# Kernel tuning notes

Hardware: AMD Instinct MI355X
Metric: run time of the kernel (lower is better)

Reference implementation:

```python
import jax, jax.numpy as jnp
import numpy as np

N, D, H, E = 8192, 1024, 4096, 8


def setup_inputs() -> dict:
    key = jax.random.key(0)
    ks = jax.random.split(key, 5)
    s_in = 1.0 / np.sqrt(D)
    s_h = 1.0 / np.sqrt(H)
    return {
        "x": jax.random.normal(ks[0], (N, D), dtype=jnp.float32),
        "Wg": jax.random.normal(ks[1], (D, E), dtype=jnp.float32) * s_in,
        "bg": jnp.zeros((E,), dtype=jnp.float32),
        "W1": jax.random.normal(ks[2], (E, D, H), dtype=jnp.float32) * s_in,
        "b1": jnp.zeros((E, H), dtype=jnp.float32),
        "W2": jax.random.normal(ks[3], (E, H, D), dtype=jnp.float32) * s_h,
        "b2": jnp.zeros((E, D), dtype=jnp.float32),
    }


def reference(x, Wg, bg, W1, b1, W2, b2):
    # gate: softmax linear router -> weights [N, E]
    weights = jax.nn.softmax(x @ Wg + bg, axis=-1)
    # all experts, batched GEMMs: h [N, E, H]
    h = jax.nn.relu(jnp.einsum("nd,edh->neh", x, W1) + b1)  # Dropout is identity at inference
    outputs = jnp.einsum("neh,ehd->ned", h, W2) + b2         # [N, E, D]
    # weighted combine over experts
    return jnp.einsum("ne,ned->nd", weights, outputs)
```

## Files before the change

kernel.cpp:

```cpp
#include <hip/hip_runtime.h>
#include <hip/hip_bf16.h>

#define DDIM 1024
#define HDIM 4096
#define NEXP 8
#define NROW 8192
#define KPAIR 8192

typedef __attribute__((ext_vector_type(8))) short s16x8;
typedef __attribute__((ext_vector_type(4))) float f32x4;

using bf16 = __hip_bfloat16;

__device__ __forceinline__ void gload16(const bf16* g, bf16* lds) {
    __builtin_amdgcn_global_load_lds(
        (const __attribute__((address_space(1))) unsigned int*)g,
        (__attribute__((address_space(3))) unsigned int*)lds,
        16, 0, 0);
}

template <int N>
__device__ __forceinline__ void wait_vmcnt() {
    if constexpr (N == 6)      asm volatile("s_waitcnt vmcnt(6)" ::: "memory");
    else if constexpr (N == 3) asm volatile("s_waitcnt vmcnt(3)" ::: "memory");
    else                       asm volatile("s_waitcnt vmcnt(0)" ::: "memory");
}

__global__ void cvtgate_kernel(const float* __restrict__ x, const float* __restrict__ Wg,
                               const float* __restrict__ bg, const float* __restrict__ b2,
                               bf16* __restrict__ xb, float* __restrict__ wts,
                               float* __restrict__ out) {
    int wave = threadIdx.x >> 6, lane = threadIdx.x & 63;
    int n = blockIdx.x * 4 + wave;
    const float* xr = x + (size_t)n * DDIM;
    bf16* xbr = xb + (size_t)n * DDIM;
    float acc[NEXP] = {0.f, 0.f, 0.f, 0.f, 0.f, 0.f, 0.f, 0.f};
#pragma unroll
    for (int j = 0; j < 4; ++j) {
        int d0 = j * 256 + lane * 4;
        float4 v = *(const float4*)&xr[d0];
        union { bf16 b[4]; uint2 u; } pk;
        pk.b[0] = __float2bfloat16(v.x);
        pk.b[1] = __float2bfloat16(v.y);
        pk.b[2] = __float2bfloat16(v.z);
        pk.b[3] = __float2bfloat16(v.w);
        *(uint2*)&xbr[d0] = pk.u;
        const float* w0 = Wg + (size_t)d0 * NEXP;
#pragma unroll
        for (int e = 0; e < NEXP; ++e)
            acc[e] += v.x * w0[e] + v.y * w0[NEXP + e] + v.z * w0[2 * NEXP + e] +
                      v.w * w0[3 * NEXP + e];
    }
#pragma unroll
    for (int off = 32; off > 0; off >>= 1) {
#pragma unroll
        for (int e = 0; e < NEXP; ++e) acc[e] += __shfl_xor(acc[e], off, 64);
    }
    float mx = -1e30f;
#pragma unroll
    for (int e = 0; e < NEXP; ++e) { acc[e] += bg[e]; mx = fmaxf(mx, acc[e]); }
    float s = 0.f;
#pragma unroll
    for (int e = 0; e < NEXP; ++e) { acc[e] = __expf(acc[e] - mx); s += acc[e]; }
    float inv = 1.0f / s;
#pragma unroll
    for (int e = 0; e < NEXP; ++e) acc[e] *= inv;
    if (lane == 0) {
#pragma unroll
        for (int e = 0; e < NEXP; ++e) wts[(size_t)n * NEXP + e] = acc[e];
    }
    float* outr = out + (size_t)n * DDIM;
#pragma unroll
    for (int j = 0; j < 4; ++j) {
        int d0 = j * 256 + lane * 4;
        float4 sum = {0.f, 0.f, 0.f, 0.f};
#pragma unroll
        for (int e = 0; e < NEXP; ++e) {
            float4 bv = *(const float4*)&b2[(size_t)e * DDIM + d0];
            sum.x += acc[e] * bv.x;
            sum.y += acc[e] * bv.y;
            sum.z += acc[e] * bv.z;
            sum.w += acc[e] * bv.w;
        }
        *(float4*)&outr[d0] = sum;
    }
}

__global__ void transpose_pair_kernel(const float* __restrict__ W1s, bf16* __restrict__ W1d,
                                      const float* __restrict__ W2s, bf16* __restrict__ W2d) {
    __shared__ float t[128][65];
    const int z = blockIdx.z;
    const float* src; bf16* dst; int C, ldo, bx, by;
    if (z < 2) {
        src = W1s + (size_t)z * DDIM * HDIM;
        dst = W1d + (size_t)z * HDIM * DDIM;
        C = HDIM; ldo = DDIM;
        bx = blockIdx.x & 31; by = blockIdx.x >> 5;
    } else {
        src = W2s + (size_t)(z - 2) * HDIM * DDIM;
        dst = W2d + (size_t)(z - 2) * HDIM;
        C = DDIM; ldo = KPAIR;
        bx = blockIdx.x & 7; by = blockIdx.x >> 3;
    }
    const int r0 = by * 64, c0 = bx * 128;
    const int tid = threadIdx.x;
    const int lrow = tid >> 5, lc4 = tid & 31;
#pragma unroll
    for (int i = 0; i < 8; ++i) {
        int rr = i * 8 + lrow;
        float4 v = *(const float4*)&src[(size_t)(r0 + rr) * C + c0 + lc4 * 4];
        t[lc4 * 4 + 0][rr] = v.x;
        t[lc4 * 4 + 1][rr] = v.y;
        t[lc4 * 4 + 2][rr] = v.z;
        t[lc4 * 4 + 3][rr] = v.w;
    }
    __syncthreads();
    const int oc = tid >> 3, oj = tid & 7;
#pragma unroll
    for (int i = 0; i < 4; ++i) {
        int c = oc + i * 32;
        union { bf16 b[8]; s16x8 v; } p;
#pragma unroll
        for (int q = 0; q < 8; ++q) p.b[q] = __float2bfloat16(t[c][oj * 8 + q]);
        *(s16x8*)&dst[(size_t)(c0 + c) * ldo + r0 + oj * 8] = p.v;
    }
}

__global__ __launch_bounds__(512, 1) void gemm1(
    const bf16* __restrict__ A, const bf16* __restrict__ BTp, bf16* __restrict__ Hsb,
    const float* __restrict__ b1p, const float* __restrict__ wts,
    int lda, int ldb, int ldc, int NT, int tilesM, int tilesN, int XGN, int e0) {
    constexpr int WROWS = 128;
    constexpr int HALFA = 256 * 32;
    constexpr int HALFB = 256 * 32;
    constexpr int ATOT = 2 * HALFA;
    constexpr int BUFE = ATOT + 2 * HALFB;
    __shared__ __align__(16) bf16 smem[2 * BUFE];

    const int tid = threadIdx.x;
    const int wave = tid >> 6, lane = tid & 63;
    const int wm = wave >> 2, wn = wave & 3;
    const int r = lane & 15, kg = lane >> 4;

    const int eh = blockIdx.x >> 9;
    const int bx = blockIdx.x & 511;
    const bf16* BT = BTp + (size_t)eh * HDIM * DDIM;
    bf16* Cout = Hsb + (size_t)eh * HDIM;
    const float* bias = b1p + (size_t)eh * HDIM;
    const int expert = e0 + eh;

    const int xcd = bx & 7, slot = bx >> 3;
    const int XGM = 8 / XGN;
    const int rm = tilesM / XGM, rn = tilesN / XGN;
    const int g = slot >> 5, u = slot & 31;
    const int gpr = rn >> 3;
    const int gm = (g / gpr) * 4 + (u >> 3);
    const int gn = (g % gpr) * 8 + (u & 7);
    const int tm = (xcd / XGN) * rm + gm;
    const int tn = (xcd % XGN) * rn + gn;

    const bf16* gA = A + (size_t)tm * 256 * lda;
    const bf16* gB = BT + (size_t)tn * 256 * ldb;

    f32x4 acc[8][4];
#pragma unroll
    for (int m = 0; m < 8; ++m)
#pragma unroll
        for (int n = 0; n < 4; ++n) acc[m][n] = (f32x4){0.f, 0.f, 0.f, 0.f};

    auto stageA = [&](int t, int ks) {
        bf16* dst = smem + (t & 1) * BUFE + ks * HALFA;
#pragma unroll
        for (int j = 0; j < 2; ++j) {
            int c = j * 512 + tid;
            int R = c >> 2, kc = (c & 3) ^ ((R >> 1) & 3);
            gload16(gA + (size_t)R * lda + t * 64 + ks * 32 + kc * 8,
                    dst + (j * 512 + wave * 64) * 8);
        }
    };
    auto stageB = [&](int t, int ks) {
        bf16* dst = smem + (t & 1) * BUFE + ATOT + ks * HALFB;
#pragma unroll
        for (int j = 0; j < 2; ++j) {
            int c = j * 512 + tid;
            int R = c >> 2, kc = (c & 3) ^ ((R >> 1) & 3);
            gload16(gB + (size_t)R * ldb + t * 64 + ks * 32 + kc * 8,
                    dst + (j * 512 + wave * 64) * 8);
        }
    };

    s16x8 aLo[4], aHi[4], bb[4];
    auto ldALo = [&](int buf, int ks) {
#pragma unroll
        for (int m = 0; m < 4; ++m) {
            int R = wm * WROWS + m * 16 + r;
            aLo[m] = *(const s16x8*)&smem[buf * BUFE + ks * HALFA + R * 32 +
                                          ((kg ^ ((R >> 1) & 3)) * 8)];
        }
    };
    auto ldAHi = [&](int buf, int ks) {
#pragma unroll
        for (int m = 0; m < 4; ++m) {
            int R = wm * WROWS + 64 + m * 16 + r;
            aHi[m] = *(const s16x8*)&smem[buf * BUFE + ks * HALFA + R * 32 +
                                          ((kg ^ ((R >> 1) & 3)) * 8)];
        }
    };
    auto ldB = [&](int buf, int ks) {
#pragma unroll
        for (int n = 0; n < 4; ++n) {
            int R = wn * 64 + n * 16 + r;
            bb[n] = *(const s16x8*)&smem[buf * BUFE + ATOT + ks * HALFB + R * 32 +
                                         ((kg ^ ((R >> 1) & 3)) * 8)];
        }
    };

    auto mfmaLo = [&]() {
#pragma unroll
        for (int m = 0; m < 4; ++m)
#pragma unroll
            for (int n = 0; n < 4; ++n)
                acc[m][n] = __builtin_amdgcn_mfma_f32_16x16x32_bf16(aLo[m], bb[n], acc[m][n], 0, 0, 0);
    };
    auto mfmaHi = [&]() {
#pragma unroll
        for (int m = 0; m < 4; ++m)
#pragma unroll
            for (int n = 0; n < 4; ++n)
                acc[4 + m][n] = __builtin_amdgcn_mfma_f32_16x16x32_bf16(aHi[m], bb[n], acc[4 + m][n], 0, 0, 0);
    };

    stageA(0, 0); stageB(0, 0); stageA(0, 1); stageB(0, 1);
    wait_vmcnt<0>();
    __builtin_amdgcn_s_barrier();

    for (int t = 0; t < NT; ++t) {
        const int b = t & 1;
        if (t + 1 < NT) { stageA(t + 1, 0); stageB(t + 1, 0); stageA(t + 1, 1); stageB(t + 1, 1); }
        ldB(b, 0); ldALo(b, 0); ldAHi(b, 0);
        asm volatile("s_waitcnt lgkmcnt(4)" ::: "memory");
        __builtin_amdgcn_sched_barrier(0);
        __builtin_amdgcn_s_setprio(1);
        mfmaLo();
        __builtin_amdgcn_s_setprio(0);
        asm volatile("s_waitcnt lgkmcnt(0)" ::: "memory");
        __builtin_amdgcn_sched_barrier(0);
        __builtin_amdgcn_s_setprio(1);
        mfmaHi();
        __builtin_amdgcn_s_setprio(0);
        ldB(b, 1); ldALo(b, 1); ldAHi(b, 1);
        asm volatile("s_waitcnt lgkmcnt(4)" ::: "memory");
        __builtin_amdgcn_sched_barrier(0);
        __builtin_amdgcn_s_setprio(1);
        mfmaLo();
        __builtin_amdgcn_s_setprio(0);
        asm volatile("s_waitcnt lgkmcnt(0)" ::: "memory");
        __builtin_amdgcn_sched_barrier(0);
        __builtin_amdgcn_s_setprio(1);
        mfmaHi();
        __builtin_amdgcn_s_setprio(0);
        if (t + 1 < NT) {
            wait_vmcnt<0>();
            __builtin_amdgcn_s_barrier();
        }
    }

    __builtin_amdgcn_s_barrier();
    bf16* hs = smem;
    const int col0 = tn * 256 + wn * 64;
#pragma unroll
    for (int n = 0; n < 4; ++n) {
        float bv = bias[col0 + n * 16 + r];
        int cl = wn * 64 + n * 16 + r;
#pragma unroll
        for (int mf = 0; mf < 8; ++mf) {
#pragma unroll
            for (int j = 0; j < 4; ++j) {
                int rl = wm * WROWS + (mf >> 2) * 64 + (mf & 3) * 16 + kg * 4 + j;
                float wv = wts[((size_t)tm * 256 + rl) * NEXP + expert];
                float v = acc[mf][n][j] + bv;
                v = v > 0.f ? v : 0.f;
                hs[rl * 256 + (cl ^ ((rl & 7) << 3))] = __float2bfloat16(wv * v);
            }
        }
    }
    __builtin_amdgcn_s_barrier();
    asm volatile("s_waitcnt lgkmcnt(0)" ::: "memory");
    const size_t rbase = (size_t)tm * 256;
    const int cbase = tn * 256;
#pragma unroll
    for (int i2 = 0; i2 < 16; ++i2) {
        int rl = wave * 32 + i2 * 2 + (lane >> 5);
        int c8 = (lane & 31) * 8;
        s16x8 v = *(const s16x8*)&hs[rl * 256 + (c8 ^ ((rl & 7) << 3))];
        *(s16x8*)&Cout[(rbase + rl) * (size_t)ldc + cbase + c8] = v;
    }
}

__global__ __launch_bounds__(256, 2) void gemm2p(
    const bf16* __restrict__ A, const bf16* __restrict__ BT, float* __restrict__ O,
    int lda, int ldb, int ldc, int NT, int tilesM, int tilesN, int XGN) {
    constexpr int HALFA = 128 * 32;
    constexpr int HALFB = 128 * 32;
    constexpr int ATOT = 2 * HALFA;
    constexpr int BUFE = ATOT + 2 * HALFB;
    constexpr int RSTR = 68;
    __shared__ __align__(16) bf16 smem[2 * BUFE];

    const int tid = threadIdx.x;
    const int wave = tid >> 6, lane = tid & 63;
    const int ksw = wave & 1, wn = wave >> 1;
    const int r = lane & 15, kg = lane >> 4;

    const int xcd = blockIdx.x & 7, slot = blockIdx.x >> 3;
    const int XGM = 8 / XGN;
    const int rm = tilesM / XGM, rn = tilesN / XGN;
    const int g = slot >> 5, u = slot & 31;
    const int gpr = rn >> 3;
    const int gm = (g / gpr) * 4 + (u >> 3);
    const int gn = (g % gpr) * 8 + (u & 7);
    const int tm = (xcd / XGN) * rm + gm;
    const int tn = (xcd % XGN) * rn + gn;

    const bf16* gA = A + (size_t)tm * 128 * lda;
    const bf16* gB = BT + (size_t)tn * 128 * ldb;

    f32x4 acc[8][4];
#pragma unroll
    for (int m = 0; m < 8; ++m)
#pragma unroll
        for (int n = 0; n < 4; ++n) acc[m][n] = (f32x4){0.f, 0.f, 0.f, 0.f};

    auto stageA_rh = [&](int t, int rh) {
        bf16* base = smem + (t & 1) * BUFE;
#pragma unroll
        for (int j = 0; j < 2; ++j) {
            int c = j * 256 + tid;
            int Rl = (c >> 2) & 63;
            int R = rh * 64 + Rl;
            int kc = (c & 3) ^ ((R >> 1) & 3);
            gload16(gA + (size_t)R * lda + t * 64 + j * 32 + kc * 8,
                    base + j * HALFA + rh * 2048 + ((c & 255) - lane) * 8 + lane * 8);
        }
    };
    auto stageB = [&](int t) {
        bf16* base = smem + (t & 1) * BUFE + ATOT;
#pragma unroll
        for (int j = 0; j < 4; ++j) {
            int c = j * 256 + tid;
            int ks = c >> 9;
            int R = (c >> 2) & 127;
            int kc = (c & 3) ^ ((R >> 1) & 3);
            gload16(gB + (size_t)R * ldb + t * 64 + ks * 32 + kc * 8,
                    base + ks * HALFB + ((c & 511) - lane) * 8 + lane * 8);
        }
    };

    s16x8 a0[4], a1[4], bfr[4];
    auto ldA0 = [&](int b) {
#pragma unroll
        for (int m = 0; m < 4; ++m) {
            int R = m * 16 + r;
            a0[m] = *(const s16x8*)&smem[b * BUFE + ksw * HALFA + R * 32 +
                                         ((kg ^ ((R >> 1) & 3)) * 8)];
        }
    };
    auto ldA1 = [&](int b) {
#pragma unroll
        for (int m = 0; m < 4; ++m) {
            int R = 64 + m * 16 + r;
            a1[m] = *(const s16x8*)&smem[b * BUFE + ksw * HALFA + R * 32 +
                                         ((kg ^ ((R >> 1) & 3)) * 8)];
        }
    };
    auto ldB = [&](int b) {
#pragma unroll
        for (int n = 0; n < 4; ++n) {
            int R = wn * 64 + n * 16 + r;
            bfr[n] = *(const s16x8*)&smem[b * BUFE + ATOT + ksw * HALFB + R * 32 +
                                          ((kg ^ ((R >> 1) & 3)) * 8)];
        }
    };

    stageA_rh(0, 0); stageA_rh(0, 1); stageB(0);
    wait_vmcnt<0>();
    __builtin_amdgcn_s_barrier();

    for (int t = 0; t < NT; ++t) {
        const int b = t & 1;
        ldB(b); ldA1(b); ldA0(b);
        if (t + 1 < NT) { stageA_rh(t + 1, 0); stageA_rh(t + 1, 1); stageB(t + 1); }
        asm volatile("s_waitcnt lgkmcnt(4)" ::: "memory");
        __builtin_amdgcn_sched_barrier(0);
        __builtin_amdgcn_s_setprio(1);
#pragma unroll
        for (int m = 0; m < 4; ++m)
#pragma unroll
            for (int n = 0; n < 4; ++n)
                acc[4 + m][n] = __builtin_amdgcn_mfma_f32_16x16x32_bf16(a1[m], bfr[n], acc[4 + m][n], 0, 0, 0);
        __builtin_amdgcn_s_setprio(0);
        asm volatile("s_waitcnt lgkmcnt(0)" ::: "memory");
        __builtin_amdgcn_sched_barrier(0);
        __builtin_amdgcn_s_setprio(1);
#pragma unroll
        for (int m = 0; m < 4; ++m)
#pragma unroll
            for (int n = 0; n < 4; ++n)
                acc[m][n] = __builtin_amdgcn_mfma_f32_16x16x32_bf16(a0[m], bfr[n], acc[m][n], 0, 0, 0);
        __builtin_amdgcn_s_setprio(0);
        if (t + 1 < NT) {
            wait_vmcnt<0>();
            __builtin_amdgcn_s_barrier();
        }
    }

    __syncthreads();
    float* red = (float*)smem;
    const int zone = wn * (64 * RSTR);
    const int col0 = tn * 128 + wn * 64;
    const size_t row0 = (size_t)tm * 128;
    if (ksw == 1) {
#pragma unroll
        for (int mq = 0; mq < 4; ++mq)
#pragma unroll
            for (int n = 0; n < 4; ++n) {
                int rl = mq * 16 + kg * 4;
                int cl = n * 16 + r;
#pragma unroll
                for (int j = 0; j < 4; ++j)
                    red[zone + (rl + j) * RSTR + cl] = acc[mq][n][j];
            }
    }
    __syncthreads();
    if (ksw == 0) {
#pragma unroll
        for (int mq = 0; mq < 4; ++mq)
#pragma unroll
            for (int j = 0; j < 4; ++j) {
                int rl = mq * 16 + kg * 4 + j;
                size_t rr = row0 + rl;
#pragma unroll
                for (int n = 0; n < 4; ++n) {
                    int cl = n * 16 + r;
                    O[rr * (size_t)ldc + col0 + cl] += acc[mq][n][j] + red[zone + rl * RSTR + cl];
                }
            }
    }
    __syncthreads();
    if (ksw == 0) {
#pragma unroll
        for (int mq = 0; mq < 4; ++mq)
#pragma unroll
            for (int n = 0; n < 4; ++n) {
                int rl = mq * 16 + kg * 4;
                int cl = n * 16 + r;
#pragma unroll
                for (int j = 0; j < 4; ++j)
                    red[zone + (rl + j) * RSTR + cl] = acc[4 + mq][n][j];
            }
    }
    __syncthreads();
    if (ksw == 1) {
#pragma unroll
        for (int mq = 0; mq < 4; ++mq)
#pragma unroll
            for (int j = 0; j < 4; ++j) {
                int rl = mq * 16 + kg * 4 + j;
                size_t rr = row0 + 64 + rl;
#pragma unroll
                for (int n = 0; n < 4; ++n) {
                    int cl = n * 16 + r;
                    O[rr * (size_t)ldc + col0 + cl] += acc[4 + mq][n][j] + red[zone + rl * RSTR + cl];
                }
            }
    }
}

extern "C" void kernel_launch(void* const* d_in, const int* in_sizes, int n_in,
                              void* d_out, int out_size, void* d_ws, size_t ws_size,
                              hipStream_t stream) {
    const float* x  = (const float*)d_in[0];
    const float* Wg = (const float*)d_in[1];
    const float* bg = (const float*)d_in[2];
    const float* W1 = (const float*)d_in[3];
    const float* b1 = (const float*)d_in[4];
    const float* W2 = (const float*)d_in[5];
    const float* b2 = (const float*)d_in[6];
    float* out = (float*)d_out;

    char* ws = (char*)d_ws;
    bf16* xb   = (bf16*)(ws);
    bf16* W1P  = (bf16*)(ws + (16ull << 20));
    bf16* W2P  = (bf16*)(ws + (32ull << 20));
    bf16* Hs   = (bf16*)(ws + (48ull << 20));
    float* wts = (float*)(ws + (176ull << 20));

    cvtgate_kernel<<<NROW / 4, 256, 0, stream>>>(x, Wg, bg, b2, xb, wts, out);

    for (int p = 0; p < 4; ++p) {
        transpose_pair_kernel<<<dim3(512, 1, 4), 256, 0, stream>>>(
            W1 + (size_t)2 * p * DDIM * HDIM, W1P,
            W2 + (size_t)2 * p * HDIM * DDIM, W2P);
        gemm1<<<1024, 512, 0, stream>>>(
            xb, W1P, Hs, b1 + (size_t)2 * p * HDIM, wts,
            DDIM, DDIM, KPAIR, DDIM / 64, 32, 16, 2, 2 * p);
        gemm2p<<<512, 256, 0, stream>>>(
            Hs, W2P, out, KPAIR, KPAIR, DDIM, KPAIR / 64, 64, 8, 1);
    }
}
```

Baseline: 1.225 ms.

## Restructure gemm1 into 128x128 tiles with intra-block split-K across wave pairs

Replaces the 256x256-tile, 512-thread gemm1 with a 128x128-tile, 256-thread kernel that runs two blocks per CU. Each pair of waves splits the K dimension of every 64-wide step, and the partial sums are reduced through LDS in the epilogue before bias, ReLU and gate scaling. LDS fragment reads now happen before the next global prefetch is issued. This aims to raise occupancy and latency hiding, at the cost of lower arithmetic intensity per tile, more global traffic and an extra LDS reduction with more barriers.

```diff
diff --git a/kernel.cpp b/kernel.cpp
--- a/kernel.cpp
+++ b/kernel.cpp
@@ -126,41 +126,38 @@
     }
 }
 
-__global__ __launch_bounds__(512, 1) void gemm1(
+__global__ __launch_bounds__(256, 2) void gemm1v3(
     const bf16* __restrict__ A, const bf16* __restrict__ BTp, bf16* __restrict__ Hsb,
-    const float* __restrict__ b1p, const float* __restrict__ wts,
-    int lda, int ldb, int ldc, int NT, int tilesM, int tilesN, int XGN, int e0) {
-    constexpr int WROWS = 128;
-    constexpr int HALFA = 256 * 32;
-    constexpr int HALFB = 256 * 32;
+    const float* __restrict__ b1p, const float* __restrict__ wts, int e0) {
+    constexpr int HALFA = 128 * 32;
+    constexpr int HALFB = 128 * 32;
     constexpr int ATOT = 2 * HALFA;
     constexpr int BUFE = ATOT + 2 * HALFB;
+    constexpr int RSTR = 68;
+    constexpr int NT = DDIM / 64;
     __shared__ __align__(16) bf16 smem[2 * BUFE];
 
     const int tid = threadIdx.x;
     const int wave = tid >> 6, lane = tid & 63;
-    const int wm = wave >> 2, wn = wave & 3;
+    const int ksw = wave & 1, wn = wave >> 1;
     const int r = lane & 15, kg = lane >> 4;
 
-    const int eh = blockIdx.x >> 9;
-    const int bx = blockIdx.x & 511;
+    const int eh = blockIdx.x >> 11;
+    const int bx = blockIdx.x & 2047;
     const bf16* BT = BTp + (size_t)eh * HDIM * DDIM;
     bf16* Cout = Hsb + (size_t)eh * HDIM;
     const float* bias = b1p + (size_t)eh * HDIM;
     const int expert = e0 + eh;
 
     const int xcd = bx & 7, slot = bx >> 3;
-    const int XGM = 8 / XGN;
-    const int rm = tilesM / XGM, rn = tilesN / XGN;
     const int g = slot >> 5, u = slot & 31;
-    const int gpr = rn >> 3;
-    const int gm = (g / gpr) * 4 + (u >> 3);
-    const int gn = (g % gpr) * 8 + (u & 7);
-    const int tm = (xcd / XGN) * rm + gm;
-    const int tn = (xcd % XGN) * rn + gn;
-
-    const bf16* gA = A + (size_t)tm * 256 * lda;
-    const bf16* gB = BT + (size_t)tn * 256 * ldb;
+    const int gm = (g >> 1) * 4 + (u >> 3);
+    const int gn = (g & 1) * 8 + (u & 7);
+    const int tm = (xcd >> 1) * 16 + gm;
+    const int tn = (xcd & 1) * 16 + gn;
+
+    const bf16* gA = A + (size_t)tm * 128 * DDIM;
+    const bf16* gB = BT + (size_t)tn * 128 * DDIM;
 
     f32x4 acc[8][4];
 #pragma unroll
@@ -168,96 +165,82 @@
 #pragma unroll
         for (int n = 0; n < 4; ++n) acc[m][n] = (f32x4){0.f, 0.f, 0.f, 0.f};
 
-    auto stageA = [&](int t, int ks) {
-        bf16* dst = smem + (t & 1) * BUFE + ks * HALFA;
+    auto stageA_rh = [&](int t, int rh) {
+        bf16* base = smem + (t & 1) * BUFE;
 #pragma unroll
         for (int j = 0; j < 2; ++j) {
-            int c = j * 512 + tid;
-            int R = c >> 2, kc = (c & 3) ^ ((R >> 1) & 3);
-            gload16(gA + (size_t)R * lda + t * 64 + ks * 32 + kc * 8,
-                    dst + (j * 512 + wave * 64) * 8);
-        }
-    };
-    auto stageB = [&](int t, int ks) {
-        bf16* dst = smem + (t & 1) * BUFE + ATOT + ks * HALFB;
-#pragma unroll
-        for (int j = 0; j < 2; ++j) {
-            int c = j * 512 + tid;
-            int R = c >> 2, kc = (c & 3) ^ ((R >> 1) & 3);
-            gload16(gB + (size_t)R * ldb + t * 64 + ks * 32 + kc * 8,
-                    dst + (j * 512 + wave * 64) * 8);
-        }
-    };
-
-    s16x8 aLo[4], aHi[4], bb[4];
-    auto ldALo = [&](int buf, int ks) {
+            int c = j * 256 + tid;
+            int Rl = (c >> 2) & 63;
+            int R = rh * 64 + Rl;
+            int kc = (c & 3) ^ ((R >> 1) & 3);
+            gload16(gA + (size_t)R * DDIM + t * 64 + j * 32 + kc * 8,
+                    base + j * HALFA + rh * 2048 + ((c & 255) - lane) * 8 + lane * 8);
+        }
+    };
+    auto stageB = [&](int t) {
+        bf16* base = smem + (t & 1) * BUFE + ATOT;
+#pragma unroll
+        for (int j = 0; j < 4; ++j) {
+            int c = j * 256 + tid;
+            int ks = c >> 9;
+            int R = (c >> 2) & 127;
+            int kc = (c & 3) ^ ((R >> 1) & 3);
+            gload16(gB + (size_t)R * DDIM + t * 64 + ks * 32 + kc * 8,
+                    base + ks * HALFB + ((c & 511) - lane) * 8 + lane * 8);
+        }
+    };
+
+    s16x8 a0[4], a1[4], bfr[4];
+    auto ldA0 = [&](int b) {
 #pragma unroll
         for (int m = 0; m < 4; ++m) {
-            int R = wm * WROWS + m * 16 + r;
-            aLo[m] = *(const s16x8*)&smem[buf * BUFE + ks * HALFA + R * 32 +
-                                          ((kg ^ ((R >> 1) & 3)) * 8)];
-        }
-    };
-    auto ldAHi = [&](int buf, int ks) {
+            int R = m * 16 + r;
+            a0[m] = *(const s16x8*)&smem[b * BUFE + ksw * HALFA + R * 32 +
+                                         ((kg ^ ((R >> 1) & 3)) * 8)];
+        }
+    };
+    auto ldA1 = [&](int b) {
 #pragma unroll
         for (int m = 0; m < 4; ++m) {
-            int R = wm * WROWS + 64 + m * 16 + r;
-            aHi[m] = *(const s16x8*)&smem[buf * BUFE + ks * HALFA + R * 32 +
-                                          ((kg ^ ((R >> 1) & 3)) * 8)];
-        }
-    };
-    auto ldB = [&](int buf, int ks) {
+            int R = 64 + m * 16 + r;
+            a1[m] = *(const s16x8*)&smem[b * BUFE + ksw * HALFA + R * 32 +
+                                         ((kg ^ ((R >> 1) & 3)) * 8)];
+        }
+    };
+    auto ldB = [&](int b) {
 #pragma unroll
         for (int n = 0; n < 4; ++n) {
             int R = wn * 64 + n * 16 + r;
-            bb[n] = *(const s16x8*)&smem[buf * BUFE + ATOT + ks * HALFB + R * 32 +
-                                         ((kg ^ ((R >> 1) & 3)) * 8)];
-        }
-    };
-
-    auto mfmaLo = [&]() {
-#pragma unroll
-        for (int m = 0; m < 4; ++m)
-#pragma unroll
-            for (int n = 0; n < 4; ++n)
-                acc[m][n] = __builtin_amdgcn_mfma_f32_16x16x32_bf16(aLo[m], bb[n], acc[m][n], 0, 0, 0);
-    };
-    auto mfmaHi = [&]() {
-#pragma unroll
-        for (int m = 0; m < 4; ++m)
-#pragma unroll
-            for (int n = 0; n < 4; ++n)
-                acc[4 + m][n] = __builtin_amdgcn_mfma_f32_16x16x32_bf16(aHi[m], bb[n], acc[4 + m][n], 0, 0, 0);
-    };
-
-    stageA(0, 0); stageB(0, 0); stageA(0, 1); stageB(0, 1);
+            bfr[n] = *(const s16x8*)&smem[b * BUFE + ATOT + ksw * HALFB + R * 32 +
+                                          ((kg ^ ((R >> 1) & 3)) * 8)];
+        }
+    };
+
+    stageA_rh(0, 0); stageA_rh(0, 1); stageB(0);
     wait_vmcnt<0>();
     __builtin_amdgcn_s_barrier();
 
     for (int t = 0; t < NT; ++t) {
         const int b = t & 1;
-        if (t + 1 < NT) { stageA(t + 1, 0); stageB(t + 1, 0); stageA(t + 1, 1); stageB(t + 1, 1); }
-        ldB(b, 0); ldALo(b, 0); ldAHi(b, 0);
+        ldB(b); ldA1(b); ldA0(b);
+        if (t + 1 < NT) { stageA_rh(t + 1, 0); stageA_rh(t + 1, 1); stageB(t + 1); }
         asm volatile("s_waitcnt lgkmcnt(4)" ::: "memory");
         __builtin_amdgcn_sched_barrier(0);
         __builtin_amdgcn_s_setprio(1);
-        mfmaLo();
+#pragma unroll
+        for (int m = 0; m < 4; ++m)
+#pragma unroll
+            for (int n = 0; n < 4; ++n)
+                acc[4 + m][n] = __builtin_amdgcn_mfma_f32_16x16x32_bf16(a1[m], bfr[n], acc[4 + m][n], 0, 0, 0);
         __builtin_amdgcn_s_setprio(0);
         asm volatile("s_waitcnt lgkmcnt(0)" ::: "memory");
         __builtin_amdgcn_sched_barrier(0);
         __builtin_amdgcn_s_setprio(1);
-        mfmaHi();
-        __builtin_amdgcn_s_setprio(0);
-        ldB(b, 1); ldALo(b, 1); ldAHi(b, 1);
-        asm volatile("s_waitcnt lgkmcnt(4)" ::: "memory");
-        __builtin_amdgcn_sched_barrier(0);
-        __builtin_amdgcn_s_setprio(1);
-        mfmaLo();
-        __builtin_amdgcn_s_setprio(0);
-        asm volatile("s_waitcnt lgkmcnt(0)" ::: "memory");
-        __builtin_amdgcn_sched_barrier(0);
-        __builtin_amdgcn_s_setprio(1);
-        mfmaHi();
+#pragma unroll
+        for (int m = 0; m < 4; ++m)
+#pragma unroll
+            for (int n = 0; n < 4; ++n)
+                acc[m][n] = __builtin_amdgcn_mfma_f32_16x16x32_bf16(a0[m], bfr[n], acc[m][n], 0, 0, 0);
         __builtin_amdgcn_s_setprio(0);
         if (t + 1 < NT) {
             wait_vmcnt<0>();
@@ -265,35 +248,90 @@
         }
     }
 
-    __builtin_amdgcn_s_barrier();
-    bf16* hs = smem;
-    const int col0 = tn * 256 + wn * 64;
-#pragma unroll
-    for (int n = 0; n < 4; ++n) {
-        float bv = bias[col0 + n * 16 + r];
-        int cl = wn * 64 + n * 16 + r;
-#pragma unroll
-        for (int mf = 0; mf < 8; ++mf) {
+    __syncthreads();
+    float* red = (float*)smem;
+    bf16* hsb = smem + 17408;
+    const int zone = wn * (64 * RSTR);
+    const size_t rowg = (size_t)tm * 128;
+    const int colg = tn * 128;
+
+    if (ksw == 1) {
+#pragma unroll
+        for (int mq = 0; mq < 4; ++mq)
+#pragma unroll
+            for (int n = 0; n < 4; ++n) {
+                int rl = mq * 16 + kg * 4;
+                int cl = n * 16 + r;
+#pragma unroll
+                for (int j = 0; j < 4; ++j)
+                    red[zone + (rl + j) * RSTR + cl] = acc[mq][n][j];
+            }
+    }
+    __syncthreads();
+    if (ksw == 0) {
+#pragma unroll
+        for (int mq = 0; mq < 4; ++mq)
 #pragma unroll
             for (int j = 0; j < 4; ++j) {
-                int rl = wm * WROWS + (mf >> 2) * 64 + (mf & 3) * 16 + kg * 4 + j;
-                float wv = wts[((size_t)tm * 256 + rl) * NEXP + expert];
-                float v = acc[mf][n][j] + bv;
-                v = v > 0.f ? v : 0.f;
-                hs[rl * 256 + (cl ^ ((rl & 7) << 3))] = __float2bfloat16(wv * v);
-            }
-        }
-    }
-    __builtin_amdgcn_s_barrier();
-    asm volatile("s_waitcnt lgkmcnt(0)" ::: "memory");
-    const size_t rbase = (size_t)tm * 256;
-    const int cbase = tn * 256;
-#pragma unroll
-    for (int i2 = 0; i2 < 16; ++i2) {
-        int rl = wave * 32 + i2 * 2 + (lane >> 5);
-        int c8 = (lane & 31) * 8;
-        s16x8 v = *(const s16x8*)&hs[rl * 256 + (c8 ^ ((rl & 7) << 3))];
-        *(s16x8*)&Cout[(rbase + rl) * (size_t)ldc + cbase + c8] = v;
+                int rl = mq * 16 + kg * 4 + j;
+                float wv = wts[(rowg + rl) * NEXP + expert];
+#pragma unroll
+                for (int n = 0; n < 4; ++n) {
+                    int cl = n * 16 + r;
+                    float v = acc[mq][n][j] + red[zone + rl * RSTR + cl] +
+                              bias[colg + wn * 64 + cl];
+                    v = v > 0.f ? v : 0.f;
+                    hsb[rl * 128 + wn * 64 + cl] = __float2bfloat16(wv * v);
+                }
+            }
+    }
+    __syncthreads();
+    {
+#pragma unroll
+        for (int i = 0; i < 4; ++i) {
+            int rl = i * 16 + (tid >> 4);
+            int c8 = (tid & 15) * 8;
+            *(s16x8*)&Cout[(rowg + rl) * (size_t)KPAIR + colg + c8] =
+                *(const s16x8*)&hsb[rl * 128 + c8];
+        }
+    }
+    if (ksw == 0) {
+#pragma unroll
+        for (int mq = 0; mq < 4; ++mq)
+#pragma unroll
+            for (int n = 0; n < 4; ++n) {
+                int rl = mq * 16 + kg * 4;
+                int cl = n * 16 + r;
+#pragma unroll
+                for (int j = 0; j < 4; ++j)
+                    red[zone + (rl + j) * RSTR + cl] = acc[4 + mq][n][j];
+            }
+    }
+    __syncthreads();
+    if (ksw == 1) {
+#pragma unroll
+        for (int mq = 0; mq < 4; ++mq)
+#pragma unroll
+            for (int j = 0; j < 4; ++j) {
+                int rl = mq * 16 + kg * 4 + j;
+                float wv = wts[(rowg + 64 + rl) * NEXP + expert];
+#pragma unroll
+                for (int n = 0; n < 4; ++n) {
+                    int cl = n * 16 + r;
+                    float v = acc[4 + mq][n][j] + red[zone + rl * RSTR + cl] +
+                              bias[colg + wn * 64 + cl];
+                    v = v > 0.f ? v : 0.f;
+                    hsb[rl * 128 + wn * 64 + cl] = __float2bfloat16(wv * v);
+                }
+            }
+    }
+    __syncthreads();
+#pragma unroll
+    for (int i = 0; i < 4; ++i) {
+        int rl = i * 16 + (tid >> 4);
+        int c8 = (tid & 15) * 8;
+        *(s16x8*)&Cout[(rowg + 64 + rl) * (size_t)KPAIR + colg + c8] =
+            *(const s16x8*)&hsb[rl * 128 + c8];
     }
 }
 
@@ -501,9 +539,8 @@
         transpose_pair_kernel<<<dim3(512, 1, 4), 256, 0, stream>>>(
             W1 + (size_t)2 * p * DDIM * HDIM, W1P,
             W2 + (size_t)2 * p * HDIM * DDIM, W2P);
-        gemm1<<<1024, 512, 0, stream>>>(
-            xb, W1P, Hs, b1 + (size_t)2 * p * HDIM, wts,
-            DDIM, DDIM, KPAIR, DDIM / 64, 32, 16, 2, 2 * p);
+        gemm1v3<<<4096, 256, 0, stream>>>(
+            xb, W1P, Hs, b1 + (size_t)2 * p * HDIM, wts, 2 * p);
         gemm2p<<<512, 256, 0, stream>>>(
             Hs, W2P, out, KPAIR, KPAIR, DDIM, KPAIR / 64, 64, 8, 1);
     }
```

Measured after the change: 1.364 ms. 11.4% more time.
